# Optimization experiments

Hardware: AMD Instinct MI355X
Metric: run time of the kernel (lower is better)

## Reference

```python
import jax, jax.numpy as jnp
import numpy as np
import math

B, S, H = 4, 1024, 768
NH = 12
HD = H // NH
MAX_POS = 1024

def setup_inputs() -> dict:
    key = jax.random.key(0)
    ks = jax.random.split(key, 8)
    sd = 1.0 / math.sqrt(H)
    return {
        "hidden_states": jax.random.normal(ks[0], (B, S, H), dtype=jnp.float32),
        "attention_mask": jnp.zeros((B, 1, 1, S), dtype=jnp.float32),
        "relative_attention_mask": jax.random.uniform(ks[1], (B, S, S), dtype=jnp.float32),
        "Wq": jax.random.normal(ks[2], (H, H), dtype=jnp.float32) * sd,
        "bq": jnp.zeros((H,), dtype=jnp.float32),
        "Wk": jax.random.normal(ks[3], (H, H), dtype=jnp.float32) * sd,
        "bk": jnp.zeros((H,), dtype=jnp.float32),
        "Wv": jax.random.normal(ks[4], (H, H), dtype=jnp.float32) * sd,
        "bv": jnp.zeros((H,), dtype=jnp.float32),
        "dist_emb": jax.random.normal(ks[5], (2 * MAX_POS - 1, HD), dtype=jnp.float32) * 0.02,
    }

def reference(hidden_states, attention_mask, relative_attention_mask,
              Wq, bq, Wk, bk, Wv, bv, dist_emb):
    b, s, h = hidden_states.shape
    def heads(x):  # [b,s,h] -> [b,nh,s,hd]
        return x.reshape(b, s, NH, HD).transpose(0, 2, 1, 3)
    q = heads(hidden_states @ Wq + bq)
    k = heads(hidden_states @ Wk + bk)
    v = heads(hidden_states @ Wv + bv)

    scores = jnp.einsum('bhld,bhrd->bhlr', q, k)

    # relative_key_query positional bias
    pos = jnp.arange(s)
    distance = pos[:, None] - pos[None, :] + MAX_POS - 1  # [s,s]
    pe = dist_emb[distance]  # [s,s,hd]
    scores = scores + jnp.einsum('bhld,lrd->bhlr', q, pe) \
                    + jnp.einsum('bhrd,lrd->bhlr', k, pe)

    scores = scores / math.sqrt(HD)
    # log-clamped relative attention mask bias
    scores = scores + jnp.log(jnp.clip(relative_attention_mask[:, None], 1e-5))
    scores = scores + attention_mask

    probs = jax.nn.softmax(scores, axis=-1)
    ctx = jnp.einsum('bhlr,bhrd->bhld', probs, v)
    return ctx.transpose(0, 2, 1, 3).reshape(b, s, h)
```

## Files before the change

### kernel.cpp

```cpp
#include <hip/hip_runtime.h>

#define DI __device__ __forceinline__

typedef __attribute__((ext_vector_type(8))) short bf16x8;
typedef __attribute__((ext_vector_type(4))) float f32x4;
typedef __attribute__((address_space(1))) const unsigned char GAS;
typedef __attribute__((address_space(3))) unsigned char LAS;

DI unsigned short f2bf(float x) {
  unsigned int u = __builtin_bit_cast(unsigned int, x);
  u = u + 0x7fffu + ((u >> 16) & 1u);
  return (unsigned short)(u >> 16);
}
DI float bf2f(unsigned short h) {
  unsigned int u = ((unsigned int)h) << 16;
  return __builtin_bit_cast(float, u);
}

__global__ __launch_bounds__(256) void prep_kernel(
    const float* __restrict__ hs, const float* __restrict__ Wq,
    const float* __restrict__ Wk, const float* __restrict__ Wv,
    const float* __restrict__ de, const float* __restrict__ rmask,
    unsigned short* __restrict__ Xb,
    unsigned short* __restrict__ Wt,
    unsigned short* __restrict__ Eb,
    _Float16* __restrict__ Lm)
{
  const int bid = blockIdx.x, t = threadIdx.x;
  __shared__ unsigned short wlds[64 * 68];
  if (bid < 1536) {
    size_t base = (size_t)bid * 2048 + (size_t)t * 8;
    float4 a = *(const float4*)(hs + base);
    float4 b = *(const float4*)(hs + base + 4);
    union { unsigned short u[8]; uint4 v; } pk;
    pk.u[0]=f2bf(a.x); pk.u[1]=f2bf(a.y); pk.u[2]=f2bf(a.z); pk.u[3]=f2bf(a.w);
    pk.u[4]=f2bf(b.x); pk.u[5]=f2bf(b.y); pk.u[6]=f2bf(b.z); pk.u[7]=f2bf(b.w);
    *(uint4*)(Xb + base) = pk.v;
  } else if (bid < 1968) {
    int q = bid - 1536;
    int wi = q / 144, tile = q % 144;
    int tr = tile / 12, tc = tile % 12;
    int k0 = tr * 64, n0 = tc * 64;
    const float* W = wi == 0 ? Wq : (wi == 1 ? Wk : Wv);
    int i = t >> 2, cb = (t & 3) * 16;
    const float* src = W + (size_t)(k0 + i) * 768 + n0 + cb;
#pragma unroll
    for (int c4 = 0; c4 < 4; ++c4) {
      float4 v = *(const float4*)(src + c4 * 4);
      wlds[i * 68 + cb + c4 * 4 + 0] = f2bf(v.x);
      wlds[i * 68 + cb + c4 * 4 + 1] = f2bf(v.y);
      wlds[i * 68 + cb + c4 * 4 + 2] = f2bf(v.z);
      wlds[i * 68 + cb + c4 * 4 + 3] = f2bf(v.w);
    }
    __syncthreads();
    int n = t >> 2, ks = (t & 3) * 16;
    union { unsigned short u[16]; uint4 v[2]; } pk;
#pragma unroll
    for (int e = 0; e < 16; ++e) pk.u[e] = wlds[(ks + e) * 68 + n];
    unsigned short* dst = Wt + (size_t)wi * 589824 + (size_t)(n0 + n) * 768 + k0 + ks;
    *(uint4*)(dst) = pk.v[0];
    *(uint4*)(dst + 8) = pk.v[1];
  } else if (bid < 2032) {
    int q = bid - 1968;
    size_t base = (size_t)q * 2048 + (size_t)t * 8;
    union { unsigned short u[8]; uint4 v; } pk;
    if (base < 131008) {
      float4 a = *(const float4*)(de + base);
      float4 b = *(const float4*)(de + base + 4);
      pk.u[0]=f2bf(a.x); pk.u[1]=f2bf(a.y); pk.u[2]=f2bf(a.z); pk.u[3]=f2bf(a.w);
      pk.u[4]=f2bf(b.x); pk.u[5]=f2bf(b.y); pk.u[6]=f2bf(b.z); pk.u[7]=f2bf(b.w);
    } else {
      pk.v = uint4{0u, 0u, 0u, 0u};
    }
    *(uint4*)(Eb + base) = pk.v;
  } else {
    int q = bid - 2032;
    size_t base = (size_t)q * 2048 + (size_t)t * 8;
    float4 a = *(const float4*)(rmask + base);
    float4 b = *(const float4*)(rmask + base + 4);
    union { _Float16 h[8]; uint4 v; } pk;
    pk.h[0] = (_Float16)__log2f(fmaxf(a.x, 1e-5f));
    pk.h[1] = (_Float16)__log2f(fmaxf(a.y, 1e-5f));
    pk.h[2] = (_Float16)__log2f(fmaxf(a.z, 1e-5f));
    pk.h[3] = (_Float16)__log2f(fmaxf(a.w, 1e-5f));
    pk.h[4] = (_Float16)__log2f(fmaxf(b.x, 1e-5f));
    pk.h[5] = (_Float16)__log2f(fmaxf(b.y, 1e-5f));
    pk.h[6] = (_Float16)__log2f(fmaxf(b.z, 1e-5f));
    pk.h[7] = (_Float16)__log2f(fmaxf(b.w, 1e-5f));
    *(uint4*)(Lm + base) = pk.v;
  }
}

__global__ __launch_bounds__(256) void proj_kernel(
    const unsigned short* __restrict__ Xb, const unsigned short* __restrict__ Wt,
    const float* __restrict__ bq, const float* __restrict__ bk, const float* __restrict__ bv,
    unsigned short* __restrict__ Qb, unsigned short* __restrict__ Kb,
    unsigned short* __restrict__ Vb)
{
  const int x = blockIdx.x, y = blockIdx.y;
  const int t = threadIdx.x, w = t >> 6, lane = t & 63, g = lane >> 4, ln = lane & 15;
  const int wm = w >> 1, wn = w & 1;
  __shared__ __align__(16) unsigned char smem[32768];
  unsigned char* sA = smem;
  unsigned char* sB = smem + 16384;
  const int m0 = x * 128, n0 = y * 128;
  const int sec = y / 6, hb = (y % 6) * 2 + wn;
  const float* bias = sec == 0 ? bq : (sec == 1 ? bk : bv);
  unsigned short* Out = sec == 0 ? Qb : (sec == 1 ? Kb : Vb);
  const unsigned char* Xbb = (const unsigned char*)Xb;
  const unsigned char* Wtb = (const unsigned char*)Wt;

  f32x4 acc[4][4];
#pragma unroll
  for (int a = 0; a < 4; ++a)
#pragma unroll
    for (int c = 0; c < 4; ++c) acc[a][c] = f32x4{0.f, 0.f, 0.f, 0.f};

  for (int kt = 0; kt < 12; ++kt) {
    __syncthreads();
#pragma unroll
    for (int ci = 0; ci < 4; ++ci) {
      int idx = ci * 1024 + lane * 16;
      int rl = idx >> 7, col = idx & 127;
      int row = w * 32 + rl;
      int scol = col ^ ((row & 7) << 4);
      __builtin_amdgcn_global_load_lds(
          (const GAS*)(Xbb + (size_t)(m0 + row) * 1536 + kt * 128 + scol),
          (LAS*)(sA + w * 4096 + ci * 1024), 16, 0, 0);
      __builtin_amdgcn_global_load_lds(
          (const GAS*)(Wtb + (size_t)(n0 + row) * 1536 + kt * 128 + scol),
          (LAS*)(sB + w * 4096 + ci * 1024), 16, 0, 0);
    }
    __syncthreads();
    bf16x8 af[4][2], bfr[4][2];
#pragma unroll
    for (int ms = 0; ms < 4; ++ms) {
      int row = wm * 64 + ms * 16 + ln;
#pragma unroll
      for (int ks = 0; ks < 2; ++ks)
        af[ms][ks] = *(const bf16x8*)(sA + ((row * 128 + ks * 64 + g * 16) ^ ((row & 7) << 4)));
    }
#pragma unroll
    for (int c = 0; c < 4; ++c) {
      int row = wn * 64 + c * 16 + ln;
#pragma unroll
      for (int ks = 0; ks < 2; ++ks)
        bfr[c][ks] = *(const bf16x8*)(sB + ((row * 128 + ks * 64 + g * 16) ^ ((row & 7) << 4)));
    }
#pragma unroll
    for (int ms = 0; ms < 4; ++ms)
#pragma unroll
      for (int c = 0; c < 4; ++c) {
        acc[ms][c] = __builtin_amdgcn_mfma_f32_16x16x32_bf16(af[ms][0], bfr[c][0], acc[ms][c], 0, 0, 0);
        acc[ms][c] = __builtin_amdgcn_mfma_f32_16x16x32_bf16(af[ms][1], bfr[c][1], acc[ms][c], 0, 0, 0);
      }
  }
  float b4[4];
#pragma unroll
  for (int c = 0; c < 4; ++c) b4[c] = bias[hb * 64 + c * 16 + ln];
#pragma unroll
  for (int ms = 0; ms < 4; ++ms)
#pragma unroll
    for (int c = 0; c < 4; ++c)
#pragma unroll
      for (int jj = 0; jj < 4; ++jj) {
        int m = m0 + wm * 64 + ms * 16 + g * 4 + jj;
        int bb = m >> 10, s = m & 1023;
        float v = acc[ms][c][jj] + b4[c];
        Out[((size_t)(bb * 12 + hb) * 1024 + s) * 64 + c * 16 + ln] = f2bf(v);
      }
}

__global__ __launch_bounds__(256) void vtrans_kernel(
    const unsigned short* __restrict__ Vb, unsigned short* __restrict__ Vtb)
{
  const int s0 = blockIdx.x * 256, bh = blockIdx.y, t = threadIdx.x;
  __shared__ __align__(16) unsigned short lds[256 * 64];
  const unsigned short* src = Vb + ((size_t)bh * 1024 + s0 + t) * 64;
#pragma unroll
  for (int gi = 0; gi < 8; ++gi) {
    uint4 v = *(const uint4*)(src + gi * 8);
    *(uint4*)((unsigned char*)lds + t * 128 + ((gi ^ (t & 7)) << 4)) = v;
  }
  __syncthreads();
  const int d = t >> 2, seg = t & 3;
  unsigned short* dst = Vtb + ((size_t)bh * 64 + d) * 1024 + s0 + seg * 64;
#pragma unroll
  for (int ck = 0; ck < 8; ++ck) {
    union { unsigned short u[8]; uint4 v; } pk;
#pragma unroll
    for (int e = 0; e < 8; ++e) {
      int sl = seg * 64 + ck * 8 + e;
      pk.u[e] = lds[sl * 64 + (((d >> 3) ^ (sl & 7)) << 3) + (d & 7)];
    }
    *(uint4*)(dst + ck * 8) = pk.v;
  }
}

__global__ __launch_bounds__(256, 2) void attn_kernel(
    const float* __restrict__ amask, const _Float16* __restrict__ Lm,
    const unsigned short* __restrict__ Qb, const unsigned short* __restrict__ Kb,
    const unsigned short* __restrict__ Vtb, const unsigned short* __restrict__ Eb,
    float* __restrict__ pctx, float* __restrict__ pm)
{
  const int orig = blockIdx.x;
  const int wg = (orig & 7) * 192 + (orig >> 3);
  const int h = wg % 12;
  const int grp = wg / 12;
  const int half = grp & 1, lb = (grp >> 1) & 15, b = grp >> 5;
  const int bh = b * 12 + h, l0 = lb * 64;
  const int t = threadIdx.x, w = t >> 6, lane = t & 63, g = lane >> 4, ln = lane & 15;
  __shared__ __align__(16) unsigned char smem[46848];
  unsigned char* sK = smem;
  unsigned char* sV = smem + 8192;
  unsigned short* Ht = (unsigned short*)(smem + 16384);
  unsigned short* Gtw = (unsigned short*)(smem + 33792 + w * 3264);
  unsigned char* Pw = (unsigned char*)Gtw;

  const unsigned short* Qrow = Qb + ((size_t)bh * 1024 + l0 + w * 16 + ln) * 64;
  const bf16x8 qa0 = *(const bf16x8*)(Qrow + g * 8);
  const bf16x8 qa1 = *(const bf16x8*)(Qrow + 32 + g * 8);

  f32x4 ctx[4];
#pragma unroll
  for (int c = 0; c < 4; ++c) ctx[c] = f32x4{0.f, 0.f, 0.f, 0.f};
  float mrun[4] = {-1e30f, -1e30f, -1e30f, -1e30f};
  float sig[4] = {0.f, 0.f, 0.f, 0.f};

  const unsigned char* Kbase = (const unsigned char*)(Kb + (size_t)bh * 65536);
  const unsigned char* Vbase = (const unsigned char*)(Vtb + (size_t)bh * 65536);
  const int itBeg = half * 8, itEnd = itBeg + 8;

  const int sp = t * 16, srow = sp >> 7, scol = sp & 127;
  uint4 kp[2], vp[2];
#pragma unroll
  for (int i = 0; i < 2; ++i) {
    kp[i] = *(const uint4*)(Kbase + (size_t)(itBeg * 64 + srow + i * 32) * 128 + scol);
    vp[i] = *(const uint4*)(Vbase + (size_t)(srow + i * 32) * 2048 + itBeg * 128 + scol);
  }

  for (int it = itBeg; it < itEnd; ++it) {
    const int r0 = it * 64;
    __syncthreads();
#pragma unroll
    for (int i = 0; i < 2; ++i) {
      int p = i * 4096 + sp, row = p >> 7;
      int ad = p ^ ((row & 7) << 4);
      *(uint4*)(sK + ad) = kp[i];
      *(uint4*)(sV + ad) = vp[i];
    }
    if (it + 1 < itEnd) {
#pragma unroll
      for (int i = 0; i < 2; ++i) {
        kp[i] = *(const uint4*)(Kbase + (size_t)(r0 + 64 + srow + i * 32) * 128 + scol);
        vp[i] = *(const uint4*)(Vbase + (size_t)(srow + i * 32) * 2048 + (r0 + 64) * 2 + scol);
      }
    }
    float lmf[4][4];
    const _Float16* lrow = Lm + (size_t)b * 1048576 + (size_t)(l0 + w * 16 + g * 4) * 1024 + r0;
#pragma unroll
    for (int jj = 0; jj < 4; ++jj)
#pragma unroll
      for (int ct = 0; ct < 4; ++ct)
        lmf[ct][jj] = (float)lrow[(size_t)jj * 1024 + ct * 16 + ln];
    float am4[4];
#pragma unroll
    for (int ct = 0; ct < 4; ++ct)
      am4[ct] = amask[b * 1024 + r0 + ct * 16 + ln] * 1.4426950408889634f;

    const int D0 = l0 - r0 + 960;
#pragma unroll
    for (int cc = 0; cc < 5; ++cc) {
      int c = w + cc;
      const unsigned short* Erow = Eb + (size_t)(D0 + c * 16 + ln) * 64;
      bf16x8 e0 = *(const bf16x8*)(Erow + g * 8);
      bf16x8 e1 = *(const bf16x8*)(Erow + 32 + g * 8);
      f32x4 ga = f32x4{0.f, 0.f, 0.f, 0.f};
      ga = __builtin_amdgcn_mfma_f32_16x16x32_bf16(qa0, e0, ga, 0, 0, 0);
      ga = __builtin_amdgcn_mfma_f32_16x16x32_bf16(qa1, e1, ga, 0, 0, 0);
      ushort4 pk = {f2bf(ga[0]), f2bf(ga[1]), f2bf(ga[2]), f2bf(ga[3])};
      *(ushort4*)(Gtw + (cc * 16 + ln) * 20 + g * 4) = pk;
    }
    __syncthreads();
    bf16x8 kb[4][2];
#pragma unroll
    for (int c = 0; c < 4; ++c)
#pragma unroll
      for (int ks = 0; ks < 2; ++ks) {
        int row = c * 16 + ln;
        kb[c][ks] = *(const bf16x8*)(sK + ((row * 128 + ks * 64 + g * 16) ^ ((row & 7) << 4)));
      }
    bf16x8 ha0, ha1;
    {
      int row = w * 16 + ln;
      ha0 = *(const bf16x8*)(sK + ((row * 128 + g * 16) ^ ((row & 7) << 4)));
      ha1 = *(const bf16x8*)(sK + ((row * 128 + 64 + g * 16) ^ ((row & 7) << 4)));
    }
#pragma unroll
    for (int cc = 0; cc < 5; ++cc) {
      int c = 3 - w + cc;
      const unsigned short* Erow = Eb + (size_t)(D0 + c * 16 + ln) * 64;
      bf16x8 e0 = *(const bf16x8*)(Erow + g * 8);
      bf16x8 e1 = *(const bf16x8*)(Erow + 32 + g * 8);
      f32x4 hac = f32x4{0.f, 0.f, 0.f, 0.f};
      hac = __builtin_amdgcn_mfma_f32_16x16x32_bf16(ha0, e0, hac, 0, 0, 0);
      hac = __builtin_amdgcn_mfma_f32_16x16x32_bf16(ha1, e1, hac, 0, 0, 0);
      ushort4 pk = {f2bf(hac[0]), f2bf(hac[1]), f2bf(hac[2]), f2bf(hac[3])};
      *(ushort4*)(Ht + (size_t)(c * 16 + ln) * 68 + w * 16 + g * 4) = pk;
    }
    __syncthreads();
    f32x4 sacc[4];
#pragma unroll
    for (int ct = 0; ct < 4; ++ct) {
      int rlb = ct * 16 + ln;
      f32x4 si;
#pragma unroll
      for (int jj = 0; jj < 4; ++jj) {
        int lloc = g * 4 + jj;
        int j = w * 16 + lloc - rlb + 63;
        si[jj] = bf2f(Gtw[(lloc - rlb + 63) * 20 + lloc]) + bf2f(Ht[(size_t)j * 68 + rlb]);
      }
      sacc[ct] = si;
      sacc[ct] = __builtin_amdgcn_mfma_f32_16x16x32_bf16(qa0, kb[ct][0], sacc[ct], 0, 0, 0);
      sacc[ct] = __builtin_amdgcn_mfma_f32_16x16x32_bf16(qa1, kb[ct][1], sacc[ct], 0, 0, 0);
    }
    float sv[4][4], rmax[4];
#pragma unroll
    for (int jj = 0; jj < 4; ++jj) {
#pragma unroll
      for (int ct = 0; ct < 4; ++ct)
        sv[ct][jj] = sacc[ct][jj] * 0.1803368801f + am4[ct] + lmf[ct][jj];
      float rv = fmaxf(fmaxf(sv[0][jj], sv[1][jj]), fmaxf(sv[2][jj], sv[3][jj]));
#pragma unroll
      for (int mm = 1; mm < 16; mm <<= 1) rv = fmaxf(rv, __shfl_xor(rv, mm));
      rmax[jj] = rv;
    }
    float sf[4], mnew[4];
#pragma unroll
    for (int jj = 0; jj < 4; ++jj) {
      mnew[jj] = fmaxf(mrun[jj], rmax[jj]);
      sf[jj] = __builtin_amdgcn_exp2f(mrun[jj] - mnew[jj]);
      mrun[jj] = mnew[jj];
    }
    float rs[4] = {0.f, 0.f, 0.f, 0.f};
    unsigned short pb[4][4];
#pragma unroll
    for (int ct = 0; ct < 4; ++ct)
#pragma unroll
      for (int jj = 0; jj < 4; ++jj) {
        float p = __builtin_amdgcn_exp2f(sv[ct][jj] - mnew[jj]);
        rs[jj] += p;
        pb[ct][jj] = f2bf(p);
      }
#pragma unroll
    for (int jj = 0; jj < 4; ++jj) {
      float rv = rs[jj];
#pragma unroll
      for (int mm = 1; mm < 16; mm <<= 1) rv += __shfl_xor(rv, mm);
      sig[jj] = sig[jj] * sf[jj] + rv;
    }
#pragma unroll
    for (int c = 0; c < 4; ++c)
#pragma unroll
      for (int jj = 0; jj < 4; ++jj) ctx[c][jj] *= sf[jj];
#pragma unroll
    for (int ct = 0; ct < 4; ++ct)
#pragma unroll
      for (int jj = 0; jj < 4; ++jj) {
        int lp = g * 4 + jj;
        *(unsigned short*)(Pw + ((lp * 128 + (ct * 16 + ln) * 2) ^ ((lp & 7) << 4))) = pb[ct][jj];
      }
    bf16x8 pa0, pa1;
    {
      int lr = ln;
      pa0 = *(const bf16x8*)(Pw + ((lr * 128 + g * 16) ^ ((lr & 7) << 4)));
      pa1 = *(const bf16x8*)(Pw + ((lr * 128 + 64 + g * 16) ^ ((lr & 7) << 4)));
    }
#pragma unroll
    for (int cd = 0; cd < 4; ++cd) {
      int row = cd * 16 + ln;
      bf16x8 v0 = *(const bf16x8*)(sV + ((row * 128 + g * 16) ^ ((row & 7) << 4)));
      bf16x8 v1 = *(const bf16x8*)(sV + ((row * 128 + 64 + g * 16) ^ ((row & 7) << 4)));
      ctx[cd] = __builtin_amdgcn_mfma_f32_16x16x32_bf16(pa0, v0, ctx[cd], 0, 0, 0);
      ctx[cd] = __builtin_amdgcn_mfma_f32_16x16x32_bf16(pa1, v1, ctx[cd], 0, 0, 0);
    }
  }
  const size_t rowb = (size_t)(half * 48 + bh) * 1024 + l0 + w * 16;
#pragma unroll
  for (int cd = 0; cd < 4; ++cd)
#pragma unroll
    for (int jj = 0; jj < 4; ++jj)
      pctx[(rowb + g * 4 + jj) * 64 + cd * 16 + ln] = ctx[cd][jj];
  if (ln == 0) {
#pragma unroll
    for (int jj = 0; jj < 4; ++jj) {
      size_t rr = rowb + g * 4 + jj;
      pm[rr * 2] = mrun[jj];
      pm[rr * 2 + 1] = sig[jj];
    }
  }
}

__global__ __launch_bounds__(256) void combine_kernel(
    const float* __restrict__ pctx, const float* __restrict__ pm,
    float* __restrict__ out)
{
  int tid = blockIdx.x * 256 + threadIdx.x;
  int row = tid >> 4, dq = (tid & 15) * 4;
  int bh = row >> 10, l = row & 1023, b = bh / 12, hh = bh % 12;
  float m0 = pm[(size_t)row * 2], s0 = pm[(size_t)row * 2 + 1];
  float m1 = pm[(size_t)(49152 + row) * 2], s1 = pm[(size_t)(49152 + row) * 2 + 1];
  float M = fmaxf(m0, m1);
  float w0 = __builtin_amdgcn_exp2f(m0 - M), w1 = __builtin_amdgcn_exp2f(m1 - M);
  float inv = 1.f / (s0 * w0 + s1 * w1);
  float4 c0 = *(const float4*)(pctx + (size_t)row * 64 + dq);
  float4 c1 = *(const float4*)(pctx + (size_t)(49152 + row) * 64 + dq);
  float4 o;
  o.x = (c0.x * w0 + c1.x * w1) * inv;
  o.y = (c0.y * w0 + c1.y * w1) * inv;
  o.z = (c0.z * w0 + c1.z * w1) * inv;
  o.w = (c0.w * w0 + c1.w * w1) * inv;
  *(float4*)(out + (size_t)(b * 1024 + l) * 768 + hh * 64 + dq) = o;
}

extern "C" void kernel_launch(void* const* d_in, const int* in_sizes, int n_in,
                              void* d_out, int out_size, void* d_ws, size_t ws_size,
                              hipStream_t stream) {
  const float* hs    = (const float*)d_in[0];
  const float* amask = (const float*)d_in[1];
  const float* rmask = (const float*)d_in[2];
  const float* Wq    = (const float*)d_in[3];
  const float* bq    = (const float*)d_in[4];
  const float* Wk    = (const float*)d_in[5];
  const float* bk    = (const float*)d_in[6];
  const float* Wv    = (const float*)d_in[7];
  const float* bv    = (const float*)d_in[8];
  const float* de    = (const float*)d_in[9];
  unsigned char* ws = (unsigned char*)d_ws;
  float*          pctx = (float*)(ws + 0);
  unsigned short* Xb   = (unsigned short*)(ws + 0);
  unsigned short* Wt   = (unsigned short*)(ws + 6291456);
  unsigned short* Vb   = (unsigned short*)(ws + 9830400);
  unsigned short* Eb   = (unsigned short*)(ws + 25165824);
  unsigned short* Qb   = (unsigned short*)(ws + 25427968);
  unsigned short* Kb   = (unsigned short*)(ws + 31719424);
  unsigned short* Vtb  = (unsigned short*)(ws + 38010880);
  _Float16*       Lm   = (_Float16*)(ws + 44302336);
  float*          pm   = (float*)(ws + 52690944);
  float* out = (float*)d_out;

  hipLaunchKernelGGL(prep_kernel, dim3(4080), dim3(256), 0, stream,
                     hs, Wq, Wk, Wv, de, rmask, Xb, Wt, Eb, Lm);
  hipLaunchKernelGGL(proj_kernel, dim3(32, 18), dim3(256), 0, stream,
                     Xb, Wt, bq, bk, bv, Qb, Kb, Vb);
  hipLaunchKernelGGL(vtrans_kernel, dim3(4, 48), dim3(256), 0, stream, Vb, Vtb);
  hipLaunchKernelGGL(attn_kernel, dim3(1536), dim3(256), 0, stream,
                     amask, Lm, Qb, Kb, Vtb, Eb, pctx, pm);
  hipLaunchKernelGGL(combine_kernel, dim3(3072), dim3(256), 0, stream, pctx, pm, out);
}
```

Measured before the change: 315.0 us.

## Restructure attention into 4-way key split with 128-row query tiles

The attention kernel now runs 512-thread blocks covering 128 query rows and splits the key range four ways instead of two. K/V tiles in LDS are shared by twice as many waves, and the H-term reuses K fragments already in registers. The additive attention mask is folded into the precomputed log-mask in prep. Row sums are computed by an MFMA against a ones vector instead of shuffle reductions, and partial contexts are stored in fp16. The combine kernel merges four partials. This adds partial-output traffic and lowers the precision of the stored partials.

```diff
diff --git a/kernel.cpp b/kernel.cpp
--- a/kernel.cpp
+++ b/kernel.cpp
@@ -21,6 +21,7 @@
     const float* __restrict__ hs, const float* __restrict__ Wq,
     const float* __restrict__ Wk, const float* __restrict__ Wv,
     const float* __restrict__ de, const float* __restrict__ rmask,
+    const float* __restrict__ amask,
     unsigned short* __restrict__ Xb,
     unsigned short* __restrict__ Wt,
     unsigned short* __restrict__ Eb,
@@ -76,17 +77,22 @@
   } else {
     int q = bid - 2032;
     size_t base = (size_t)q * 2048 + (size_t)t * 8;
+    int b = (int)(base >> 20);
+    int r = (int)(base & 1023);
     float4 a = *(const float4*)(rmask + base);
-    float4 b = *(const float4*)(rmask + base + 4);
+    float4 bb = *(const float4*)(rmask + base + 4);
+    float4 m0 = *(const float4*)(amask + b * 1024 + r);
+    float4 m1 = *(const float4*)(amask + b * 1024 + r + 4);
+    const float L2E = 1.4426950408889634f;
     union { _Float16 h[8]; uint4 v; } pk;
-    pk.h[0] = (_Float16)__log2f(fmaxf(a.x, 1e-5f));
-    pk.h[1] = (_Float16)__log2f(fmaxf(a.y, 1e-5f));
-    pk.h[2] = (_Float16)__log2f(fmaxf(a.z, 1e-5f));
-    pk.h[3] = (_Float16)__log2f(fmaxf(a.w, 1e-5f));
-    pk.h[4] = (_Float16)__log2f(fmaxf(b.x, 1e-5f));
-    pk.h[5] = (_Float16)__log2f(fmaxf(b.y, 1e-5f));
-    pk.h[6] = (_Float16)__log2f(fmaxf(b.z, 1e-5f));
-    pk.h[7] = (_Float16)__log2f(fmaxf(b.w, 1e-5f));
+    pk.h[0] = (_Float16)(__log2f(fmaxf(a.x, 1e-5f)) + m0.x * L2E);
+    pk.h[1] = (_Float16)(__log2f(fmaxf(a.y, 1e-5f)) + m0.y * L2E);
+    pk.h[2] = (_Float16)(__log2f(fmaxf(a.z, 1e-5f)) + m0.z * L2E);
+    pk.h[3] = (_Float16)(__log2f(fmaxf(a.w, 1e-5f)) + m0.w * L2E);
+    pk.h[4] = (_Float16)(__log2f(fmaxf(bb.x, 1e-5f)) + m1.x * L2E);
+    pk.h[5] = (_Float16)(__log2f(fmaxf(bb.y, 1e-5f)) + m1.y * L2E);
+    pk.h[6] = (_Float16)(__log2f(fmaxf(bb.z, 1e-5f)) + m1.z * L2E);
+    pk.h[7] = (_Float16)(__log2f(fmaxf(bb.w, 1e-5f)) + m1.w * L2E);
     *(uint4*)(Lm + base) = pk.v;
   }
 }
@@ -197,77 +203,61 @@
   }
 }
 
-__global__ __launch_bounds__(256, 2) void attn_kernel(
-    const float* __restrict__ amask, const _Float16* __restrict__ Lm,
+__global__ __launch_bounds__(512, 4) void attn_kernel(
+    const _Float16* __restrict__ Lm,
     const unsigned short* __restrict__ Qb, const unsigned short* __restrict__ Kb,
     const unsigned short* __restrict__ Vtb, const unsigned short* __restrict__ Eb,
-    float* __restrict__ pctx, float* __restrict__ pm)
+    _Float16* __restrict__ pctx, float* __restrict__ pm)
 {
   const int orig = blockIdx.x;
   const int wg = (orig & 7) * 192 + (orig >> 3);
   const int h = wg % 12;
   const int grp = wg / 12;
-  const int half = grp & 1, lb = (grp >> 1) & 15, b = grp >> 5;
-  const int bh = b * 12 + h, l0 = lb * 64;
+  const int split = grp & 3, lb = (grp >> 2) & 7, b = grp >> 5;
+  const int bh = b * 12 + h, l0 = lb * 128;
   const int t = threadIdx.x, w = t >> 6, lane = t & 63, g = lane >> 4, ln = lane & 15;
-  __shared__ __align__(16) unsigned char smem[46848];
+  __shared__ __align__(16) unsigned char smem[68608];
   unsigned char* sK = smem;
   unsigned char* sV = smem + 8192;
   unsigned short* Ht = (unsigned short*)(smem + 16384);
-  unsigned short* Gtw = (unsigned short*)(smem + 33792 + w * 3264);
+  unsigned short* Gtw = (unsigned short*)(smem + 42496 + w * 3264);
   unsigned char* Pw = (unsigned char*)Gtw;
 
   const unsigned short* Qrow = Qb + ((size_t)bh * 1024 + l0 + w * 16 + ln) * 64;
   const bf16x8 qa0 = *(const bf16x8*)(Qrow + g * 8);
   const bf16x8 qa1 = *(const bf16x8*)(Qrow + 32 + g * 8);
 
-  f32x4 ctx[4];
+  bf16x8 ones;
+#pragma unroll
+  for (int i = 0; i < 8; ++i) ones[i] = (short)0x3F80;
+
+  f32x4 ctx[4], ctx5;
 #pragma unroll
   for (int c = 0; c < 4; ++c) ctx[c] = f32x4{0.f, 0.f, 0.f, 0.f};
+  ctx5 = f32x4{0.f, 0.f, 0.f, 0.f};
   float mrun[4] = {-1e30f, -1e30f, -1e30f, -1e30f};
-  float sig[4] = {0.f, 0.f, 0.f, 0.f};
 
   const unsigned char* Kbase = (const unsigned char*)(Kb + (size_t)bh * 65536);
   const unsigned char* Vbase = (const unsigned char*)(Vtb + (size_t)bh * 65536);
-  const int itBeg = half * 8, itEnd = itBeg + 8;
+  const int itBeg = split * 4, itEnd = itBeg + 4;
 
   const int sp = t * 16, srow = sp >> 7, scol = sp & 127;
-  uint4 kp[2], vp[2];
-#pragma unroll
-  for (int i = 0; i < 2; ++i) {
-    kp[i] = *(const uint4*)(Kbase + (size_t)(itBeg * 64 + srow + i * 32) * 128 + scol);
-    vp[i] = *(const uint4*)(Vbase + (size_t)(srow + i * 32) * 2048 + itBeg * 128 + scol);
-  }
+  uint4 kp, vp;
+  kp = *(const uint4*)(Kbase + (size_t)(itBeg * 64 + srow) * 128 + scol);
+  vp = *(const uint4*)(Vbase + (size_t)srow * 2048 + itBeg * 128 + scol);
 
   for (int it = itBeg; it < itEnd; ++it) {
     const int r0 = it * 64;
     __syncthreads();
-#pragma unroll
-    for (int i = 0; i < 2; ++i) {
-      int p = i * 4096 + sp, row = p >> 7;
-      int ad = p ^ ((row & 7) << 4);
-      *(uint4*)(sK + ad) = kp[i];
-      *(uint4*)(sV + ad) = vp[i];
+    {
+      int ad = sp ^ ((srow & 7) << 4);
+      *(uint4*)(sK + ad) = kp;
+      *(uint4*)(sV + ad) = vp;
     }
     if (it + 1 < itEnd) {
-#pragma unroll
-      for (int i = 0; i < 2; ++i) {
-        kp[i] = *(const uint4*)(Kbase + (size_t)(r0 + 64 + srow + i * 32) * 128 + scol);
-        vp[i] = *(const uint4*)(Vbase + (size_t)(srow + i * 32) * 2048 + (r0 + 64) * 2 + scol);
-      }
-    }
-    float lmf[4][4];
-    const _Float16* lrow = Lm + (size_t)b * 1048576 + (size_t)(l0 + w * 16 + g * 4) * 1024 + r0;
-#pragma unroll
-    for (int jj = 0; jj < 4; ++jj)
-#pragma unroll
-      for (int ct = 0; ct < 4; ++ct)
-        lmf[ct][jj] = (float)lrow[(size_t)jj * 1024 + ct * 16 + ln];
-    float am4[4];
-#pragma unroll
-    for (int ct = 0; ct < 4; ++ct)
-      am4[ct] = amask[b * 1024 + r0 + ct * 16 + ln] * 1.4426950408889634f;
-
+      kp = *(const uint4*)(Kbase + (size_t)(r0 + 64 + srow) * 128 + scol);
+      vp = *(const uint4*)(Vbase + (size_t)srow * 2048 + (r0 + 64) * 2 + scol);
+    }
     const int D0 = l0 - r0 + 960;
 #pragma unroll
     for (int cc = 0; cc < 5; ++cc) {
@@ -290,23 +280,31 @@
         int row = c * 16 + ln;
         kb[c][ks] = *(const bf16x8*)(sK + ((row * 128 + ks * 64 + g * 16) ^ ((row & 7) << 4)));
       }
-    bf16x8 ha0, ha1;
+    float lmf[4][4];
     {
-      int row = w * 16 + ln;
-      ha0 = *(const bf16x8*)(sK + ((row * 128 + g * 16) ^ ((row & 7) << 4)));
-      ha1 = *(const bf16x8*)(sK + ((row * 128 + 64 + g * 16) ^ ((row & 7) << 4)));
-    }
-#pragma unroll
-    for (int cc = 0; cc < 5; ++cc) {
-      int c = 3 - w + cc;
-      const unsigned short* Erow = Eb + (size_t)(D0 + c * 16 + ln) * 64;
-      bf16x8 e0 = *(const bf16x8*)(Erow + g * 8);
-      bf16x8 e1 = *(const bf16x8*)(Erow + 32 + g * 8);
-      f32x4 hac = f32x4{0.f, 0.f, 0.f, 0.f};
-      hac = __builtin_amdgcn_mfma_f32_16x16x32_bf16(ha0, e0, hac, 0, 0, 0);
-      hac = __builtin_amdgcn_mfma_f32_16x16x32_bf16(ha1, e1, hac, 0, 0, 0);
-      ushort4 pk = {f2bf(hac[0]), f2bf(hac[1]), f2bf(hac[2]), f2bf(hac[3])};
-      *(ushort4*)(Ht + (size_t)(c * 16 + ln) * 68 + w * 16 + g * 4) = pk;
+      const _Float16* lrow = Lm + (size_t)b * 1048576 +
+                             (size_t)(l0 + w * 16 + g * 4) * 1024 + r0;
+#pragma unroll
+      for (int jj = 0; jj < 4; ++jj)
+#pragma unroll
+        for (int ct = 0; ct < 4; ++ct)
+          lmf[ct][jj] = (float)lrow[(size_t)jj * 1024 + ct * 16 + ln];
+    }
+    {
+      const int rt = w >> 1;
+      const int kbeg = (w & 1) ? 5 : 0, kend = (w & 1) ? 9 : 5;
+#pragma unroll
+      for (int k = kbeg; k < kend; ++k) {
+        int c = 3 - rt + k;
+        const unsigned short* Erow = Eb + (size_t)(D0 + c * 16 + ln) * 64;
+        bf16x8 e0 = *(const bf16x8*)(Erow + g * 8);
+        bf16x8 e1 = *(const bf16x8*)(Erow + 32 + g * 8);
+        f32x4 hac = f32x4{0.f, 0.f, 0.f, 0.f};
+        hac = __builtin_amdgcn_mfma_f32_16x16x32_bf16(kb[rt][0], e0, hac, 0, 0, 0);
+        hac = __builtin_amdgcn_mfma_f32_16x16x32_bf16(kb[rt][1], e1, hac, 0, 0, 0);
+        ushort4 pk = {f2bf(hac[0]), f2bf(hac[1]), f2bf(hac[2]), f2bf(hac[3])};
+        *(ushort4*)(Ht + (size_t)(c * 16 + ln) * 68 + rt * 16 + g * 4) = pk;
+      }
     }
     __syncthreads();
     f32x4 sacc[4];
@@ -317,52 +315,43 @@
 #pragma unroll
       for (int jj = 0; jj < 4; ++jj) {
         int lloc = g * 4 + jj;
-        int j = w * 16 + lloc - rlb + 63;
-        si[jj] = bf2f(Gtw[(lloc - rlb + 63) * 20 + lloc]) + bf2f(Ht[(size_t)j * 68 + rlb]);
+        si[jj] = bf2f(Gtw[(lloc - rlb + 63) * 20 + lloc]) +
+                 bf2f(Ht[(size_t)(w * 16 + lloc - rlb + 63) * 68 + rlb]);
       }
       sacc[ct] = si;
       sacc[ct] = __builtin_amdgcn_mfma_f32_16x16x32_bf16(qa0, kb[ct][0], sacc[ct], 0, 0, 0);
       sacc[ct] = __builtin_amdgcn_mfma_f32_16x16x32_bf16(qa1, kb[ct][1], sacc[ct], 0, 0, 0);
     }
-    float sv[4][4], rmax[4];
+    float rmax[4];
 #pragma unroll
     for (int jj = 0; jj < 4; ++jj) {
 #pragma unroll
       for (int ct = 0; ct < 4; ++ct)
-        sv[ct][jj] = sacc[ct][jj] * 0.1803368801f + am4[ct] + lmf[ct][jj];
-      float rv = fmaxf(fmaxf(sv[0][jj], sv[1][jj]), fmaxf(sv[2][jj], sv[3][jj]));
+        sacc[ct][jj] = sacc[ct][jj] * 0.1803368801f + lmf[ct][jj];
+      float rv = fmaxf(fmaxf(sacc[0][jj], sacc[1][jj]), fmaxf(sacc[2][jj], sacc[3][jj]));
 #pragma unroll
       for (int mm = 1; mm < 16; mm <<= 1) rv = fmaxf(rv, __shfl_xor(rv, mm));
       rmax[jj] = rv;
     }
-    float sf[4], mnew[4];
+    float sf[4];
 #pragma unroll
     for (int jj = 0; jj < 4; ++jj) {
-      mnew[jj] = fmaxf(mrun[jj], rmax[jj]);
-      sf[jj] = __builtin_amdgcn_exp2f(mrun[jj] - mnew[jj]);
-      mrun[jj] = mnew[jj];
-    }
-    float rs[4] = {0.f, 0.f, 0.f, 0.f};
+      float mnew = fmaxf(mrun[jj], rmax[jj]);
+      sf[jj] = __builtin_amdgcn_exp2f(mrun[jj] - mnew);
+      mrun[jj] = mnew;
+    }
     unsigned short pb[4][4];
 #pragma unroll
     for (int ct = 0; ct < 4; ++ct)
 #pragma unroll
-      for (int jj = 0; jj < 4; ++jj) {
-        float p = __builtin_amdgcn_exp2f(sv[ct][jj] - mnew[jj]);
-        rs[jj] += p;
-        pb[ct][jj] = f2bf(p);
-      }
-#pragma unroll
-    for (int jj = 0; jj < 4; ++jj) {
-      float rv = rs[jj];
-#pragma unroll
-      for (int mm = 1; mm < 16; mm <<= 1) rv += __shfl_xor(rv, mm);
-      sig[jj] = sig[jj] * sf[jj] + rv;
-    }
+      for (int jj = 0; jj < 4; ++jj)
+        pb[ct][jj] = f2bf(__builtin_amdgcn_exp2f(sacc[ct][jj] - mrun[jj]));
 #pragma unroll
     for (int c = 0; c < 4; ++c)
 #pragma unroll
       for (int jj = 0; jj < 4; ++jj) ctx[c][jj] *= sf[jj];
+#pragma unroll
+    for (int jj = 0; jj < 4; ++jj) ctx5[jj] *= sf[jj];
 #pragma unroll
     for (int ct = 0; ct < 4; ++ct)
 #pragma unroll
@@ -384,43 +373,61 @@
       ctx[cd] = __builtin_amdgcn_mfma_f32_16x16x32_bf16(pa0, v0, ctx[cd], 0, 0, 0);
       ctx[cd] = __builtin_amdgcn_mfma_f32_16x16x32_bf16(pa1, v1, ctx[cd], 0, 0, 0);
     }
-  }
-  const size_t rowb = (size_t)(half * 48 + bh) * 1024 + l0 + w * 16;
+    ctx5 = __builtin_amdgcn_mfma_f32_16x16x32_bf16(pa0, ones, ctx5, 0, 0, 0);
+    ctx5 = __builtin_amdgcn_mfma_f32_16x16x32_bf16(pa1, ones, ctx5, 0, 0, 0);
+  }
+  const size_t rowb = (size_t)split * 49152 + (size_t)bh * 1024 + l0 + w * 16;
 #pragma unroll
   for (int cd = 0; cd < 4; ++cd)
 #pragma unroll
     for (int jj = 0; jj < 4; ++jj)
-      pctx[(rowb + g * 4 + jj) * 64 + cd * 16 + ln] = ctx[cd][jj];
+      pctx[(rowb + g * 4 + jj) * 64 + cd * 16 + ln] = (_Float16)ctx[cd][jj];
   if (ln == 0) {
 #pragma unroll
     for (int jj = 0; jj < 4; ++jj) {
       size_t rr = rowb + g * 4 + jj;
       pm[rr * 2] = mrun[jj];
-      pm[rr * 2 + 1] = sig[jj];
+      pm[rr * 2 + 1] = ctx5[jj];
     }
   }
 }
 
 __global__ __launch_bounds__(256) void combine_kernel(
-    const float* __restrict__ pctx, const float* __restrict__ pm,
+    const _Float16* __restrict__ pctx, const float* __restrict__ pm,
     float* __restrict__ out)
 {
   int tid = blockIdx.x * 256 + threadIdx.x;
-  int row = tid >> 4, dq = (tid & 15) * 4;
+  int row = tid >> 3, d0 = (tid & 7) * 8;
   int bh = row >> 10, l = row & 1023, b = bh / 12, hh = bh % 12;
-  float m0 = pm[(size_t)row * 2], s0 = pm[(size_t)row * 2 + 1];
-  float m1 = pm[(size_t)(49152 + row) * 2], s1 = pm[(size_t)(49152 + row) * 2 + 1];
-  float M = fmaxf(m0, m1);
-  float w0 = __builtin_amdgcn_exp2f(m0 - M), w1 = __builtin_amdgcn_exp2f(m1 - M);
-  float inv = 1.f / (s0 * w0 + s1 * w1);
-  float4 c0 = *(const float4*)(pctx + (size_t)row * 64 + dq);
-  float4 c1 = *(const float4*)(pctx + (size_t)(49152 + row) * 64 + dq);
-  float4 o;
-  o.x = (c0.x * w0 + c1.x * w1) * inv;
-  o.y = (c0.y * w0 + c1.y * w1) * inv;
-  o.z = (c0.z * w0 + c1.z * w1) * inv;
-  o.w = (c0.w * w0 + c1.w * w1) * inv;
-  *(float4*)(out + (size_t)(b * 1024 + l) * 768 + hh * 64 + dq) = o;
+  float m[4], s[4];
+#pragma unroll
+  for (int sp = 0; sp < 4; ++sp) {
+    size_t rr = (size_t)sp * 49152 + row;
+    m[sp] = pm[rr * 2];
+    s[sp] = pm[rr * 2 + 1];
+  }
+  float M = fmaxf(fmaxf(m[0], m[1]), fmaxf(m[2], m[3]));
+  float wv[4], denom = 0.f;
+#pragma unroll
+  for (int sp = 0; sp < 4; ++sp) {
+    wv[sp] = __builtin_amdgcn_exp2f(m[sp] - M);
+    denom += wv[sp] * s[sp];
+  }
+  float inv = 1.f / denom;
+  float o[8] = {0.f, 0.f, 0.f, 0.f, 0.f, 0.f, 0.f, 0.f};
+#pragma unroll
+  for (int sp = 0; sp < 4; ++sp) {
+    const _Float16* src = pctx + ((size_t)sp * 49152 + row) * 64 + d0;
+    union { uint4 v; _Float16 h[8]; } u;
+    u.v = *(const uint4*)src;
+#pragma unroll
+    for (int e = 0; e < 8; ++e) o[e] += wv[sp] * (float)u.h[e];
+  }
+  float* dst = out + (size_t)(b * 1024 + l) * 768 + hh * 64 + d0;
+  float4 o0 = {o[0] * inv, o[1] * inv, o[2] * inv, o[3] * inv};
+  float4 o1 = {o[4] * inv, o[5] * inv, o[6] * inv, o[7] * inv};
+  *(float4*)dst = o0;
+  *(float4*)(dst + 4) = o1;
 }
 
 extern "C" void kernel_launch(void* const* d_in, const int* in_sizes, int n_in,
@@ -437,7 +444,7 @@
   const float* bv    = (const float*)d_in[8];
   const float* de    = (const float*)d_in[9];
   unsigned char* ws = (unsigned char*)d_ws;
-  float*          pctx = (float*)(ws + 0);
+  _Float16*       pctx = (_Float16*)(ws + 0);
   unsigned short* Xb   = (unsigned short*)(ws + 0);
   unsigned short* Wt   = (unsigned short*)(ws + 6291456);
   unsigned short* Vb   = (unsigned short*)(ws + 9830400);
@@ -450,11 +457,11 @@
   float* out = (float*)d_out;
 
   hipLaunchKernelGGL(prep_kernel, dim3(4080), dim3(256), 0, stream,
-                     hs, Wq, Wk, Wv, de, rmask, Xb, Wt, Eb, Lm);
+                     hs, Wq, Wk, Wv, de, rmask, amask, Xb, Wt, Eb, Lm);
   hipLaunchKernelGGL(proj_kernel, dim3(32, 18), dim3(256), 0, stream,
                      Xb, Wt, bq, bk, bv, Qb, Kb, Vb);
   hipLaunchKernelGGL(vtrans_kernel, dim3(4, 48), dim3(256), 0, stream, Vb, Vtb);
-  hipLaunchKernelGGL(attn_kernel, dim3(1536), dim3(256), 0, stream,
-                     amask, Lm, Qb, Kb, Vtb, Eb, pctx, pm);
-  hipLaunchKernelGGL(combine_kernel, dim3(3072), dim3(256), 0, stream, pctx, pm, out);
-}
+  hipLaunchKernelGGL(attn_kernel, dim3(1536), dim3(512), 0, stream,
+                     Lm, Qb, Kb, Vtb, Eb, pctx, pm);
+  hipLaunchKernelGGL(combine_kernel, dim3(1536), dim3(256), 0, stream, pctx, pm, out);
+}
```

New measurement: 610.0 us. 1.94x slower.
